# Optimization experiments

Hardware: AMD Instinct MI355X
Metric: run time of the kernel (lower is better)

## Reference

```python
import jax, jax.numpy as jnp
import numpy as np

N, S, D = 4, 2048, 1024
H, HD = 16, 64  # heads, head_dim = patch_size // heads
SCALE = 1.0 / np.float32(np.sqrt(D))  # module divides by sqrt(patch_size), not sqrt(head_dim)


def setup_inputs() -> dict:
    key = jax.random.key(0)
    ks = jax.random.split(key, 8)
    return {
        "values": jax.random.normal(ks[0], (N, S, D), dtype=jnp.float32),
        "keys": jax.random.normal(ks[1], (N, S, D), dtype=jnp.float32),
        "query": jax.random.normal(ks[2], (N, S, D), dtype=jnp.float32),
        "Wv": jax.random.normal(ks[3], (HD, HD), dtype=jnp.float32) / np.float32(np.sqrt(HD)),
        "Wk": jax.random.normal(ks[4], (HD, HD), dtype=jnp.float32) / np.float32(np.sqrt(HD)),
        "Wq": jax.random.normal(ks[5], (HD, HD), dtype=jnp.float32) / np.float32(np.sqrt(HD)),
        "Wo": jax.random.normal(ks[6], (D, D), dtype=jnp.float32) / np.float32(np.sqrt(D)),
        "bo": jnp.zeros((D,), dtype=jnp.float32),
    }


def reference(values, keys, query, Wv, Wk, Wq, Wo, bo):
    n, ql = query.shape[0], query.shape[1]
    # reshape to heads, then per-head shared linear projections (torch Linear: x @ W.T)
    v = jnp.einsum('nlhd,ed->nlhe', values.reshape(n, -1, H, HD), Wv)
    k = jnp.einsum('nkhd,ed->nkhe', keys.reshape(n, -1, H, HD), Wk)
    q = jnp.einsum('nqhd,ed->nqhe', query.reshape(n, -1, H, HD), Wq)
    energy = jnp.einsum('nqhd,nkhd->nhqk', q, k)  # [N,H,Sq,Sk]
    attn = jax.nn.softmax(energy * SCALE, axis=3)
    out = jnp.einsum('nhql,nlhd->nqhd', attn, v).reshape(n, ql, H * HD)
    return out @ Wo.T + bo
```

## Files before the change

### kernel.cpp

```cpp
#include <hip/hip_runtime.h>
#include <stdint.h>

typedef _Float16 f16;
typedef f16 half2_t __attribute__((ext_vector_type(2)));
typedef f16 half4_t __attribute__((ext_vector_type(4)));
typedef f16 half8_t __attribute__((ext_vector_type(8)));
typedef __fp16 fp16x2_t __attribute__((ext_vector_type(2)));
typedef float f32x4 __attribute__((ext_vector_type(4)));

#define N_ 4
#define S_ 2048
#define D_ 1024
#define H_ 16
#define HD_ 64
#define LOG2E 1.44269504088896340736f
#define SCALE_ 0.03125f

typedef __attribute__((address_space(1))) void gvoid;
typedef __attribute__((address_space(3))) void lvoid;

__device__ __forceinline__ void load_lds16(const void* g, void* l) {
  __builtin_amdgcn_global_load_lds((gvoid*)(uintptr_t)g, (lvoid*)l, 16, 0, 0);
}

__device__ __forceinline__ f32x4 mfma32(half8_t a, half8_t b, f32x4 c) {
  return __builtin_amdgcn_mfma_f32_16x16x32_f16(a, b, c, 0, 0, 0);
}

__device__ __forceinline__ half2_t pack_f16(float a, float b) {
  fp16x2_t t = __builtin_amdgcn_cvt_pkrtz(a, b);
  return __builtin_bit_cast(half2_t, t);
}

__global__ void wprep(const float* __restrict__ Wv, const float* __restrict__ Wo,
                      const float* __restrict__ Wq, const float* __restrict__ Wk,
                      f16* __restrict__ Wbig, float* __restrict__ Mq) {
  int b = blockIdx.x;
  if (b < 1024) {
    int j = b;
#pragma unroll
    for (int c = 0; c < 4; ++c) {
      int i = c * 256 + threadIdx.x;
      int h = i >> 6, dd = i & 63;
      const float* wo = Wo + (size_t)j * 1024 + h * 64;
      float acc = 0.f;
#pragma unroll 8
      for (int e = 0; e < 64; ++e) acc += Wv[e * 64 + dd] * wo[e];
      Wbig[(size_t)j * 1024 + i] = (f16)acc;
    }
  } else {
    int tid = (b - 1024) * 256 + threadIdx.x;
    int d = tid >> 6, e = tid & 63;
    float acc = 0.f;
#pragma unroll 8
    for (int r = 0; r < 64; ++r) acc += Wq[r * 64 + d] * Wk[r * 64 + e];
    Mq[d * 64 + e] = acc * (SCALE_ * LOG2E);
  }
}

__global__ __launch_bounds__(256) void prep2(const float* __restrict__ Q,
                                             const float* __restrict__ K,
                                             const float* __restrict__ V,
                                             const float* __restrict__ Mq,
                                             f16* __restrict__ q16, f16* __restrict__ k16,
                                             f16* __restrict__ v16) {
  __shared__ char smem[16384];
  int b = blockIdx.x;
  if (b < 512) {
    float* mql = (float*)smem;
#pragma unroll
    for (int c = 0; c < 16; ++c) mql[c * 256 + threadIdx.x] = Mq[c * 256 + threadIdx.x];
    __syncthreads();
    int n = b >> 7, sblk = b & 127;
    int L = threadIdx.x & 63, w = threadIdx.x >> 6;
    int lq = L & 15, hh = w * 4 + (L >> 4);
    int s = sblk * 16 + lq;
    const float* qrow = Q + ((size_t)(n * S_ + s)) * D_ + hh * HD_;
    f32x4 acc4[16];
#pragma unroll
    for (int i = 0; i < 16; ++i) acc4[i] = (f32x4){0.f, 0.f, 0.f, 0.f};
    for (int d4 = 0; d4 < 16; ++d4) {
      f32x4 qv = *(const f32x4*)(qrow + d4 * 4);
#pragma unroll
      for (int dj = 0; dj < 4; ++dj) {
        const f32x4* mrow = (const f32x4*)(mql + (d4 * 4 + dj) * 64);
        float qs = qv[dj];
#pragma unroll
        for (int i = 0; i < 16; ++i) acc4[i] += mrow[i] * qs;
      }
    }
    size_t cbase = ((size_t)((n * 16 + hh) * 128 + sblk)) * 2;
#pragma unroll
    for (int dp = 0; dp < 2; ++dp) {
#pragma unroll
      for (int qd = 0; qd < 4; ++qd) {
        half8_t hv;
        f32x4 a0 = acc4[dp * 8 + qd * 2], a1 = acc4[dp * 8 + qd * 2 + 1];
#pragma unroll
        for (int j = 0; j < 4; ++j) { hv[j] = (f16)a0[j]; hv[4 + j] = (f16)a1[j]; }
        *(half8_t*)(q16 + (cbase + dp) * 512 + (qd * 16 + lq) * 8) = hv;
      }
    }
    const float* krow = K + ((size_t)(n * S_ + s)) * D_ + hh * HD_;
    f32x4 kr[16];
#pragma unroll
    for (int i = 0; i < 16; ++i) kr[i] = *(const f32x4*)(krow + i * 4);
#pragma unroll
    for (int dp = 0; dp < 2; ++dp) {
#pragma unroll
      for (int qd = 0; qd < 4; ++qd) {
        half8_t hv;
        f32x4 a0 = kr[dp * 8 + qd * 2], a1 = kr[dp * 8 + qd * 2 + 1];
#pragma unroll
        for (int j = 0; j < 4; ++j) { hv[j] = (f16)a0[j]; hv[4 + j] = (f16)a1[j]; }
        *(half8_t*)(k16 + (cbase + dp) * 512 + (qd * 16 + lq) * 8) = hv;
      }
    }
  } else {
    f16* lv = (f16*)smem;
    int b2 = b - 512;
    int n = b2 >> 10, hh = (b2 >> 6) & 15, sb = b2 & 63;
    int t = threadIdx.x;
    {
      int r = t >> 3, ic = t & 7;
      const float* src = V + ((size_t)(n * S_ + sb * 32 + r)) * D_ + hh * HD_ + ic * 8;
      f32x4 a = *(const f32x4*)src;
      f32x4 b3 = *(const f32x4*)(src + 4);
      half8_t hv;
#pragma unroll
      for (int j = 0; j < 4; ++j) { hv[j] = (f16)a[j]; hv[4 + j] = (f16)b3[j]; }
      *(half8_t*)(lv + r * 64 + ic * 8) = hv;
    }
    __syncthreads();
    {
      int mt = t >> 6, L = t & 63;
      int quad = L >> 4, ld = L & 15;
      half8_t o;
#pragma unroll
      for (int j = 0; j < 4; ++j) {
        o[j]     = lv[(quad * 4 + j) * 64 + mt * 16 + ld];
        o[4 + j] = lv[(quad * 4 + j + 16) * 64 + mt * 16 + ld];
      }
      *(half8_t*)(v16 + (((size_t)(n * 16 + hh) * 64 + sb) * 4 + mt) * 512 + L * 8) = o;
    }
  }
}

__global__ __launch_bounds__(256, 2) void flash(const f16* __restrict__ q16,
                                                const f16* __restrict__ k16,
                                                const f16* __restrict__ v16,
                                                f16* __restrict__ att) {
  int nh = blockIdx.x;
  int qt = blockIdx.y;
  int L = threadIdx.x & 63, w = threadIdx.x >> 6;
  int lq = L & 15, quad = L >> 4;

  const half8_t* qg = (const half8_t*)q16;
  half8_t qB[4][2];
#pragma unroll
  for (int j = 0; j < 4; ++j) {
    size_t qc = ((size_t)(nh * 128 + qt * 16 + w * 4 + j)) * 2;
    qB[j][0] = qg[qc * 64 + L];
    qB[j][1] = qg[(qc + 1) * 64 + L];
  }

  f32x4 accO[4][4];
#pragma unroll
  for (int j = 0; j < 4; ++j)
#pragma unroll
    for (int i = 0; i < 4; ++i) accO[j][i] = (f32x4){0.f, 0.f, 0.f, 0.f};
  f32x4 lvec[4];
#pragma unroll
  for (int j = 0; j < 4; ++j) lvec[j] = (f32x4){0.f, 0.f, 0.f, 0.f};

  const char* kg = (const char*)k16 + (size_t)nh * 262144 + L * 16;
  const char* vg = (const char*)v16 + (size_t)nh * 262144 + L * 16;

  for (int it = 0; it < 32; ++it) {
    const char* kb = kg + (size_t)it * 8192;
    const char* vb = vg + (size_t)it * 8192;
    half8_t kf[8], vf8[8];
#pragma unroll
    for (int c = 0; c < 8; ++c) kf[c] = *(const half8_t*)(kb + c * 1024);
#pragma unroll
    for (int c = 0; c < 8; ++c) vf8[c] = *(const half8_t*)(vb + c * 1024);
#pragma unroll
    for (int g = 0; g < 2; ++g) {
      half4_t pcg[4][2];
#pragma unroll
      for (int u = 0; u < 2; ++u) {
        int mt = 2 * g + u;
        half8_t k0 = kf[mt * 2 + 0];
        half8_t k1 = kf[mt * 2 + 1];
#pragma unroll
        for (int j = 0; j < 4; ++j) {
          f32x4 a = (f32x4){0.f, 0.f, 0.f, 0.f};
          __builtin_amdgcn_s_setprio(1);
          a = mfma32(k0, qB[j][0], a);
          a = mfma32(k1, qB[j][1], a);
          __builtin_amdgcn_s_setprio(0);
          f32x4 p;
#pragma unroll
          for (int r = 0; r < 4; ++r) p[r] = __builtin_amdgcn_exp2f(a[r]);
          lvec[j] += p;
          half2_t c01 = pack_f16(p[0], p[1]);
          half2_t c23 = pack_f16(p[2], p[3]);
          pcg[j][u] = __builtin_shufflevector(c01, c23, 0, 1, 2, 3);
        }
      }
      half8_t pb[4];
#pragma unroll
      for (int j = 0; j < 4; ++j)
        pb[j] = __builtin_shufflevector(pcg[j][0], pcg[j][1], 0, 1, 2, 3, 4, 5, 6, 7);
      __builtin_amdgcn_s_setprio(1);
#pragma unroll
      for (int mt2 = 0; mt2 < 4; ++mt2) {
        half8_t vf = vf8[g * 4 + mt2];
#pragma unroll
        for (int j = 0; j < 4; ++j)
          accO[j][mt2] = mfma32(vf, pb[j], accO[j][mt2]);
      }
      __builtin_amdgcn_s_setprio(0);
    }
  }

  int n = nh >> 4, h = nh & 15;
#pragma unroll
  for (int j = 0; j < 4; ++j) {
    float l = lvec[j][0] + lvec[j][1] + lvec[j][2] + lvec[j][3];
    l += __shfl_xor(l, 16, 64);
    l += __shfl_xor(l, 32, 64);
    float inv_l = 1.0f / l;
    int s = qt * 256 + w * 64 + j * 16 + lq;
    f16* orow = att + ((size_t)(n * S_ + s)) * D_ + h * HD_;
#pragma unroll
    for (int mt2 = 0; mt2 < 4; ++mt2) {
      half4_t o;
#pragma unroll
      for (int r = 0; r < 4; ++r) o[r] = (f16)(accO[j][mt2][r] * inv_l);
      *(half4_t*)(orow + mt2 * 16 + quad * 4) = o;
    }
  }
}

__global__ __launch_bounds__(256, 2) void ogemm(const f16* __restrict__ A, const f16* __restrict__ Bm,
                                                const float* __restrict__ bias, float* __restrict__ C) {
  __shared__ char lds[32768];
  int bm = blockIdx.x, bn = blockIdx.y;
  int L = threadIdx.x & 63, w = threadIdx.x >> 6;
  int wm = w >> 1, wn = w & 1;
  int lq = L & 15, quad = L >> 4;
  int lr = L >> 2, lc = L & 3;
  int src_c = lc ^ (lr & 3);
  f32x4 acc[16];
#pragma unroll
  for (int i = 0; i < 16; ++i) acc[i] = (f32x4){0.f, 0.f, 0.f, 0.f};

  const f16* ga0 = A + ((size_t)(bm * 128 + (w * 2) * 16 + lr)) * 1024 + src_c * 8;
  const f16* gb0 = Bm + ((size_t)(bn * 128 + (w * 2) * 16 + lr)) * 1024 + src_c * 8;

#pragma unroll
  for (int t = 0; t < 2; ++t)
#pragma unroll
    for (int c = 0; c < 2; ++c) {
      load_lds16(ga0 + t * 32 + (size_t)c * 16 * 1024, lds + t * 16384 + (w * 2 + c) * 1024);
      load_lds16(gb0 + t * 32 + (size_t)c * 16 * 1024, lds + t * 16384 + 8192 + (w * 2 + c) * 1024);
    }
  __syncthreads();

  for (int kt = 0; kt < 32; ++kt) {
    const char* base = lds + (kt & 1) * 16384;
    half8_t af[4], bf[4];
#pragma unroll
    for (int t = 0; t < 4; ++t) {
      int ch = quad ^ (lq & 3);
      af[t] = *(const half8_t*)(base + (wm * 64 + t * 16 + lq) * 64 + ch * 16);
      bf[t] = *(const half8_t*)(base + 8192 + (wn * 64 + t * 16 + lq) * 64 + ch * 16);
    }
#pragma unroll
    for (int mt = 0; mt < 4; ++mt)
#pragma unroll
      for (int nt = 0; nt < 4; ++nt)
        acc[mt * 4 + nt] =
            __builtin_amdgcn_mfma_f32_16x16x32_f16(af[mt], bf[nt], acc[mt * 4 + nt], 0, 0, 0);
    __syncthreads();
    if (kt + 2 < 32) {
      char* dst = lds + (kt & 1) * 16384;
#pragma unroll
      for (int c = 0; c < 2; ++c) {
        load_lds16(ga0 + (kt + 2) * 32 + (size_t)c * 16 * 1024, dst + (w * 2 + c) * 1024);
        load_lds16(gb0 + (kt + 2) * 32 + (size_t)c * 16 * 1024, dst + 8192 + (w * 2 + c) * 1024);
      }
    }
  }

#pragma unroll
  for (int nt = 0; nt < 4; ++nt) {
    int col = bn * 128 + wn * 64 + nt * 16 + lq;
    float bv = bias[col];
#pragma unroll
    for (int mt = 0; mt < 4; ++mt) {
#pragma unroll
      for (int r = 0; r < 4; ++r) {
        int row = bm * 128 + wm * 64 + mt * 16 + quad * 4 + r;
        C[(size_t)row * 1024 + col] = acc[mt * 4 + nt][r] + bv;
      }
    }
  }
}

extern "C" void kernel_launch(void* const* d_in, const int* in_sizes, int n_in,
                              void* d_out, int out_size, void* d_ws, size_t ws_size,
                              hipStream_t stream) {
  const float* V  = (const float*)d_in[0];
  const float* K  = (const float*)d_in[1];
  const float* Q  = (const float*)d_in[2];
  const float* Wv = (const float*)d_in[3];
  const float* Wk = (const float*)d_in[4];
  const float* Wq = (const float*)d_in[5];
  const float* Wo = (const float*)d_in[6];
  const float* bo = (const float*)d_in[7];
  float* out = (float*)d_out;

  char* ws = (char*)d_ws;
  float* Mq  = (float*)(ws);
  f16* Wbig  = (f16*)(ws + (1ull << 20));
  f16* q16   = (f16*)(ws + (3ull << 20));
  f16* k16   = (f16*)(ws + (19ull << 20));
  f16* v16   = (f16*)(ws + (35ull << 20));
  f16* att   = (f16*)(ws + (51ull << 20));

  wprep<<<1040, 256, 0, stream>>>(Wv, Wo, Wq, Wk, Wbig, Mq);
  prep2<<<4608, 256, 0, stream>>>(Q, K, V, Mq, q16, k16, v16);
  flash<<<dim3(64, 8), 256, 0, stream>>>(q16, k16, v16, att);
  ogemm<<<dim3(64, 8), 256, 0, stream>>>(att, Wbig, bo, out);
}
```

Before: 273.9 us.

## Halve per-wave query tiles, double flash grid, compute row sums via MFMA

The flash kernel now handles 2 query tiles per wave instead of 4, doubles the grid along the query axis, and raises launch bounds to 4 blocks per CU to cut register pressure and increase occupancy. K/V fragments are loaded per half-iteration rather than all at once, shrinking live registers further. The softmax denominator is accumulated with an MFMA against a vector of ones instead of vector adds plus cross-lane shuffles. In exchange, each K/V tile is now reloaded by twice as many waves, which raises global/L2 traffic, and the extra MFMA adds matrix-core work.

```diff
diff --git a/kernel.cpp b/kernel.cpp
--- a/kernel.cpp
+++ b/kernel.cpp
@@ -146,7 +146,7 @@
   }
 }
 
-__global__ __launch_bounds__(256, 2) void flash(const f16* __restrict__ q16,
+__global__ __launch_bounds__(256, 4) void flash(const f16* __restrict__ q16,
                                                 const f16* __restrict__ k16,
                                                 const f16* __restrict__ v16,
                                                 f16* __restrict__ att) {
@@ -156,44 +156,45 @@
   int lq = L & 15, quad = L >> 4;
 
   const half8_t* qg = (const half8_t*)q16;
-  half8_t qB[4][2];
-#pragma unroll
-  for (int j = 0; j < 4; ++j) {
-    size_t qc = ((size_t)(nh * 128 + qt * 16 + w * 4 + j)) * 2;
+  half8_t qB[2][2];
+#pragma unroll
+  for (int j = 0; j < 2; ++j) {
+    size_t qc = ((size_t)(nh * 128 + qt * 8 + w * 2 + j)) * 2;
     qB[j][0] = qg[qc * 64 + L];
     qB[j][1] = qg[(qc + 1) * 64 + L];
   }
 
-  f32x4 accO[4][4];
-#pragma unroll
-  for (int j = 0; j < 4; ++j)
+  half8_t ones;
+#pragma unroll
+  for (int i = 0; i < 8; ++i) ones[i] = (f16)1.0f;
+
+  f32x4 accO[2][4];
+#pragma unroll
+  for (int j = 0; j < 2; ++j)
 #pragma unroll
     for (int i = 0; i < 4; ++i) accO[j][i] = (f32x4){0.f, 0.f, 0.f, 0.f};
-  f32x4 lvec[4];
-#pragma unroll
-  for (int j = 0; j < 4; ++j) lvec[j] = (f32x4){0.f, 0.f, 0.f, 0.f};
+  f32x4 lsum[2] = {(f32x4){0.f, 0.f, 0.f, 0.f}, (f32x4){0.f, 0.f, 0.f, 0.f}};
 
   const char* kg = (const char*)k16 + (size_t)nh * 262144 + L * 16;
   const char* vg = (const char*)v16 + (size_t)nh * 262144 + L * 16;
 
   for (int it = 0; it < 32; ++it) {
-    const char* kb = kg + (size_t)it * 8192;
-    const char* vb = vg + (size_t)it * 8192;
-    half8_t kf[8], vf8[8];
-#pragma unroll
-    for (int c = 0; c < 8; ++c) kf[c] = *(const half8_t*)(kb + c * 1024);
-#pragma unroll
-    for (int c = 0; c < 8; ++c) vf8[c] = *(const half8_t*)(vb + c * 1024);
 #pragma unroll
     for (int g = 0; g < 2; ++g) {
-      half4_t pcg[4][2];
+      const char* kb = kg + (size_t)it * 8192 + g * 4096;
+      const char* vb = vg + (size_t)it * 8192 + g * 4096;
+      half8_t kfr[4], vfr[4];
+#pragma unroll
+      for (int c = 0; c < 4; ++c) kfr[c] = *(const half8_t*)(kb + c * 1024);
+#pragma unroll
+      for (int c = 0; c < 4; ++c) vfr[c] = *(const half8_t*)(vb + c * 1024);
+      half4_t pcg[2][2];
 #pragma unroll
       for (int u = 0; u < 2; ++u) {
-        int mt = 2 * g + u;
-        half8_t k0 = kf[mt * 2 + 0];
-        half8_t k1 = kf[mt * 2 + 1];
-#pragma unroll
-        for (int j = 0; j < 4; ++j) {
+        half8_t k0 = kfr[u * 2 + 0];
+        half8_t k1 = kfr[u * 2 + 1];
+#pragma unroll
+        for (int j = 0; j < 2; ++j) {
           f32x4 a = (f32x4){0.f, 0.f, 0.f, 0.f};
           __builtin_amdgcn_s_setprio(1);
           a = mfma32(k0, qB[j][0], a);
@@ -202,23 +203,23 @@
           f32x4 p;
 #pragma unroll
           for (int r = 0; r < 4; ++r) p[r] = __builtin_amdgcn_exp2f(a[r]);
-          lvec[j] += p;
           half2_t c01 = pack_f16(p[0], p[1]);
           half2_t c23 = pack_f16(p[2], p[3]);
           pcg[j][u] = __builtin_shufflevector(c01, c23, 0, 1, 2, 3);
         }
       }
-      half8_t pb[4];
-#pragma unroll
-      for (int j = 0; j < 4; ++j)
+      half8_t pb[2];
+#pragma unroll
+      for (int j = 0; j < 2; ++j)
         pb[j] = __builtin_shufflevector(pcg[j][0], pcg[j][1], 0, 1, 2, 3, 4, 5, 6, 7);
       __builtin_amdgcn_s_setprio(1);
 #pragma unroll
+      for (int j = 0; j < 2; ++j) lsum[j] = mfma32(ones, pb[j], lsum[j]);
+#pragma unroll
       for (int mt2 = 0; mt2 < 4; ++mt2) {
-        half8_t vf = vf8[g * 4 + mt2];
-#pragma unroll
-        for (int j = 0; j < 4; ++j)
-          accO[j][mt2] = mfma32(vf, pb[j], accO[j][mt2]);
+#pragma unroll
+        for (int j = 0; j < 2; ++j)
+          accO[j][mt2] = mfma32(vfr[mt2], pb[j], accO[j][mt2]);
       }
       __builtin_amdgcn_s_setprio(0);
     }
@@ -226,12 +227,9 @@
 
   int n = nh >> 4, h = nh & 15;
 #pragma unroll
-  for (int j = 0; j < 4; ++j) {
-    float l = lvec[j][0] + lvec[j][1] + lvec[j][2] + lvec[j][3];
-    l += __shfl_xor(l, 16, 64);
-    l += __shfl_xor(l, 32, 64);
-    float inv_l = 1.0f / l;
-    int s = qt * 256 + w * 64 + j * 16 + lq;
+  for (int j = 0; j < 2; ++j) {
+    float inv_l = 1.0f / lsum[j][0];
+    int s = qt * 128 + (w * 2 + j) * 16 + lq;
     f16* orow = att + ((size_t)(n * S_ + s)) * D_ + h * HD_;
 #pragma unroll
     for (int mt2 = 0; mt2 < 4; ++mt2) {
@@ -332,6 +330,6 @@
 
   wprep<<<1040, 256, 0, stream>>>(Wv, Wo, Wq, Wk, Wbig, Mq);
   prep2<<<4608, 256, 0, stream>>>(Q, K, V, Mq, q16, k16, v16);
-  flash<<<dim3(64, 8), 256, 0, stream>>>(q16, k16, v16, att);
+  flash<<<dim3(64, 16), 256, 0, stream>>>(q16, k16, v16, att);
   ogemm<<<dim3(64, 8), 256, 0, stream>>>(att, Wbig, bo, out);
 }
```

After: 278.0 us. Within noise of the previous version (+1.5%).

## Software-pipeline attention loop so QK MFMA overlaps exp/pack of previous chunk

Applied to the files above, without the earlier changes.

Restructures the attention inner loop into 64 half-chunks, where each step runs the QK MFMAs for the next chunk and the PV MFMAs for the previous one before doing exp2 and packing. K and V fragment loads are issued one step ahead. The goal is to hide the transcendental/VALU latency and the global load latency behind matrix-core work. The extra live registers (aQK, pb, prefetched fragments) may raise VGPR pressure and lower occupancy.

```diff
diff --git a/kernel.cpp b/kernel.cpp
--- a/kernel.cpp
+++ b/kernel.cpp
@@ -176,53 +176,87 @@
   const char* kg = (const char*)k16 + (size_t)nh * 262144 + L * 16;
   const char* vg = (const char*)v16 + (size_t)nh * 262144 + L * 16;
 
-  for (int it = 0; it < 32; ++it) {
-    const char* kb = kg + (size_t)it * 8192;
-    const char* vb = vg + (size_t)it * 8192;
-    half8_t kf[8], vf8[8];
-#pragma unroll
-    for (int c = 0; c < 8; ++c) kf[c] = *(const half8_t*)(kb + c * 1024);
-#pragma unroll
-    for (int c = 0; c < 8; ++c) vf8[c] = *(const half8_t*)(vb + c * 1024);
-#pragma unroll
-    for (int g = 0; g < 2; ++g) {
-      half4_t pcg[4][2];
-#pragma unroll
-      for (int u = 0; u < 2; ++u) {
-        int mt = 2 * g + u;
-        half8_t k0 = kf[mt * 2 + 0];
-        half8_t k1 = kf[mt * 2 + 1];
-#pragma unroll
-        for (int j = 0; j < 4; ++j) {
-          f32x4 a = (f32x4){0.f, 0.f, 0.f, 0.f};
-          __builtin_amdgcn_s_setprio(1);
-          a = mfma32(k0, qB[j][0], a);
-          a = mfma32(k1, qB[j][1], a);
-          __builtin_amdgcn_s_setprio(0);
-          f32x4 p;
-#pragma unroll
-          for (int r = 0; r < 4; ++r) p[r] = __builtin_amdgcn_exp2f(a[r]);
-          lvec[j] += p;
-          half2_t c01 = pack_f16(p[0], p[1]);
-          half2_t c23 = pack_f16(p[2], p[3]);
-          pcg[j][u] = __builtin_shufflevector(c01, c23, 0, 1, 2, 3);
-        }
-      }
-      half8_t pb[4];
-#pragma unroll
-      for (int j = 0; j < 4; ++j)
-        pb[j] = __builtin_shufflevector(pcg[j][0], pcg[j][1], 0, 1, 2, 3, 4, 5, 6, 7);
-      __builtin_amdgcn_s_setprio(1);
-#pragma unroll
-      for (int mt2 = 0; mt2 < 4; ++mt2) {
-        half8_t vf = vf8[g * 4 + mt2];
-#pragma unroll
-        for (int j = 0; j < 4; ++j)
-          accO[j][mt2] = mfma32(vf, pb[j], accO[j][mt2]);
-      }
-      __builtin_amdgcn_s_setprio(0);
-    }
-  }
+  half8_t kfA[4], vfA[4], pb[4];
+  f32x4 aQK[2][4];
+
+#define QK16(KF)                                              \
+  {                                                           \
+    __builtin_amdgcn_s_setprio(1);                            \
+    _Pragma("unroll")                                         \
+    for (int u = 0; u < 2; ++u) {                             \
+      _Pragma("unroll")                                       \
+      for (int j = 0; j < 4; ++j) {                           \
+        f32x4 a = (f32x4){0.f, 0.f, 0.f, 0.f};                \
+        a = mfma32(KF[u * 2], qB[j][0], a);                   \
+        a = mfma32(KF[u * 2 + 1], qB[j][1], a);               \
+        aQK[u][j] = a;                                        \
+      }                                                       \
+    }                                                         \
+    __builtin_amdgcn_s_setprio(0);                            \
+  }
+
+#define PV16(VF)                                              \
+  {                                                           \
+    __builtin_amdgcn_s_setprio(1);                            \
+    _Pragma("unroll")                                         \
+    for (int mt2 = 0; mt2 < 4; ++mt2) {                       \
+      _Pragma("unroll")                                       \
+      for (int j = 0; j < 4; ++j)                             \
+        accO[j][mt2] = mfma32(VF[mt2], pb[j], accO[j][mt2]);  \
+    }                                                         \
+    __builtin_amdgcn_s_setprio(0);                            \
+  }
+
+#define EXPPACK                                                             \
+  {                                                                         \
+    half4_t pc[2][4];                                                       \
+    _Pragma("unroll")                                                       \
+    for (int u = 0; u < 2; ++u) {                                           \
+      _Pragma("unroll")                                                     \
+      for (int j = 0; j < 4; ++j) {                                         \
+        f32x4 p;                                                            \
+        _Pragma("unroll")                                                   \
+        for (int r = 0; r < 4; ++r) p[r] = __builtin_amdgcn_exp2f(aQK[u][j][r]); \
+        lvec[j] += p;                                                       \
+        pc[u][j] = __builtin_shufflevector(pack_f16(p[0], p[1]),            \
+                                           pack_f16(p[2], p[3]), 0, 1, 2, 3); \
+      }                                                                     \
+    }                                                                       \
+    _Pragma("unroll")                                                       \
+    for (int j = 0; j < 4; ++j)                                             \
+      pb[j] = __builtin_shufflevector(pc[0][j], pc[1][j], 0, 1, 2, 3, 4, 5, 6, 7); \
+  }
+
+#pragma unroll
+  for (int c = 0; c < 4; ++c) {
+    kfA[c] = *(const half8_t*)(kg + c * 1024);
+    vfA[c] = *(const half8_t*)(vg + c * 1024);
+  }
+  QK16(kfA);
+#pragma unroll
+  for (int c = 0; c < 4; ++c) kfA[c] = *(const half8_t*)(kg + 4096 + c * 1024);
+  EXPPACK;
+
+  for (int gg = 1; gg < 64; ++gg) {
+    QK16(kfA);
+    PV16(vfA);
+    if (gg + 1 < 64) {
+      const char* kb = kg + (size_t)(gg + 1) * 4096;
+#pragma unroll
+      for (int c = 0; c < 4; ++c) kfA[c] = *(const half8_t*)(kb + c * 1024);
+    }
+    {
+      const char* vb = vg + (size_t)gg * 4096;
+#pragma unroll
+      for (int c = 0; c < 4; ++c) vfA[c] = *(const half8_t*)(vb + c * 1024);
+    }
+    EXPPACK;
+  }
+  PV16(vfA);
+
+#undef QK16
+#undef PV16
+#undef EXPPACK
 
   int n = nh >> 4, h = nh & 15;
 #pragma unroll
```

Result: no change. 269.5 us (-1.6%).
